# Performance work log

Measured on AMD Instinct MI355X. Metric: run time of the kernel, lower is better.

## Reference

```python
import jax, jax.numpy as jnp
import numpy as np

B, S, F, D, K = 4096, 64, 8, 64, 16  # batch_size, seq_len, input_size, d_model, knns


def setup_inputs() -> dict:
    key = jax.random.key(0)
    ks = jax.random.split(key, 3)
    return {
        "x": jax.random.normal(ks[0], (B, S, F), jnp.float32),
        "W_emb": jax.random.normal(ks[1], (F, D), jnp.float32) / np.sqrt(F),
        "b_emb": jnp.zeros((D,), jnp.float32),
        "W_proj": jax.random.normal(ks[2], (D, F), jnp.float32) / np.sqrt(D),
        "b_proj": jnp.zeros((F,), jnp.float32),
    }


def reference(x, W_emb, b_emb, W_proj, b_proj):
    # enc_embedding
    x_enc = x @ W_emb + b_emb                       # [B,S,D]
    x_re = x_enc.reshape(B, S * D)                  # flatten per sample
    # batch self-similarity
    attn = jnp.einsum('bl,cl->bc', x_re, x_re) / np.sqrt(D * S)
    diag = jnp.eye(B, dtype=bool)
    attn = jnp.where(diag, -jnp.inf, attn)
    scores = jax.nn.softmax(attn, axis=-1)          # [B,B]
    # einsum('bd,bc->bd', x_re, scores) == x_re * scores.sum(-1)
    x_rec = x_re * jnp.sum(scores, axis=-1, keepdims=True)
    x_rec = x_rec.reshape(B, S, D)
    x_rec_proj = x_rec @ W_proj + b_proj            # [B,S,F]
    # top-k neighbor gather
    _, top_idx = jax.lax.top_k(scores, K)           # [B,K] int32
    gathered = x_rec_proj[top_idx]                  # [B,K,S,F]
    diff_1 = jnp.mean(jnp.diff(gathered, axis=1) ** 2)
    diff_2 = jnp.mean(jnp.diff(gathered, axis=2) ** 2)
    loss = jnp.mean((x_rec_proj - x) ** 2) + diff_1 + diff_2  # var == 2
    return loss, x_rec_proj
```

## Files before the change

### kernel.cpp

```cpp
#include <hip/hip_runtime.h>
#include <math.h>

#define NB 4096
#define NS 64
#define NF 8
#define ND 64
#define KL 512
#define NK 16

typedef _Float16 half8 __attribute__((ext_vector_type(8)));
typedef float    f32x4 __attribute__((ext_vector_type(4)));

#define GLD16(src, dst) \
  __builtin_amdgcn_global_load_lds((const __attribute__((address_space(1))) void*)(src), \
                                   (__attribute__((address_space(3))) void*)(dst), 16, 0, 0)

#define WAITVM(N) asm volatile("s_waitcnt vmcnt(" #N ")" ::: "memory")

__device__ __forceinline__ unsigned short f2bf_rne(float f) {
    unsigned v = __float_as_uint(f);
    return (unsigned short)((v + 0x7FFFu + ((v >> 16) & 1u)) >> 16);
}
__device__ __forceinline__ unsigned bf16key(float v, int col) {
    const unsigned u = f2bf_rne(v);
    const unsigned s = (u & 0x8000u) ? (~u & 0xFFFFu) : (u | 0x8000u);
    return (s << 12) | (unsigned)(4095 - col);
}

#define UPD2(M1, M2, K) { const unsigned k_ = (K); \
    if (k_ > M1) { M2 = M1; M1 = k_; } else if (k_ > M2) M2 = k_; }

__device__ __forceinline__ float blk_reduce(float v, float* red) {
    #pragma unroll
    for (int o = 32; o > 0; o >>= 1) v += __shfl_down(v, o, 64);
    const int t = threadIdx.x;
    __syncthreads();
    if ((t & 63) == 0) red[t >> 6] = v;
    __syncthreads();
    float r = 0.f;
    if (t == 0) r = red[0] + red[1] + red[2] + red[3];
    return r;
}

__global__ __launch_bounds__(64) void consts_kernel(
    const float* __restrict__ Wemb, const float* __restrict__ bemb,
    const float* __restrict__ Wp, const float* __restrict__ bp,
    float* __restrict__ cst, double* __restrict__ acc)
{
    __shared__ float sWe[NF * ND];
    __shared__ float sWp[ND * NF];
    __shared__ float sbe[ND];
    __shared__ float sbp[NF];
    const int t = threadIdx.x;
    #pragma unroll
    for (int i = 0; i < 12; ++i) acc[t + i * 64] = 0.0;
    #pragma unroll
    for (int i = 0; i < 8; ++i) { sWe[t + i * 64] = Wemb[t + i * 64]; sWp[t + i * 64] = Wp[t + i * 64]; }
    sbe[t] = bemb[t];
    if (t < NF) sbp[t] = bp[t];
    __syncthreads();
    const int f = t >> 3, f2 = t & 7;
    float g = 0.f, m = 0.f;
    #pragma unroll
    for (int d = 0; d < ND; ++d) {
        g += sWe[f * ND + d] * sWe[f2 * ND + d];
        m += sWe[f * ND + d] * sWp[d * NF + f2];
    }
    cst[t] = g;
    cst[64 + t] = m;
    if (t < NF) {
        float uu = 0.f, cc = 0.f;
        #pragma unroll
        for (int d = 0; d < ND; ++d) {
            uu += sWe[t * ND + d] * sbe[d];
            cc += sbe[d] * sWp[d * NF + t];
        }
        cst[128 + t] = uu;
        cst[136 + t] = cc + sbp[t];
    }
}

__global__ __launch_bounds__(256) void prep_kernel(
    const float* __restrict__ x, const float* __restrict__ cst,
    _Float16* __restrict__ X16, _Float16* __restrict__ Y16,
    float* __restrict__ proj, float* __restrict__ r, double* __restrict__ acc)
{
    __shared__ float sG[64], sM[64], su[8], sc[8];
    __shared__ float red[4];
    const int t = threadIdx.x, lane = t & 63, w = t >> 6;
    if (t < 64) sG[t] = cst[t];
    else if (t < 128) sM[t - 64] = cst[t];
    else if (t < 136) su[t - 128] = cst[t];
    else if (t < 144) sc[t - 136] = cst[t];
    __syncthreads();
    const int b = blockIdx.x * 4 + w;
    const size_t base = (size_t)b * KL + lane * 8;
    const f32x4 x0 = *(const f32x4*)&x[base];
    const f32x4 x1 = *(const f32x4*)&x[base + 4];
    float xv[8] = {x0[0], x0[1], x0[2], x0[3], x1[0], x1[1], x1[2], x1[3]};
    float yv[8], pv[8];
    #pragma unroll
    for (int f2 = 0; f2 < 8; ++f2) { yv[f2] = 0.f; pv[f2] = sc[f2]; }
    #pragma unroll
    for (int f = 0; f < 8; ++f)
        #pragma unroll
        for (int f2 = 0; f2 < 8; ++f2) {
            yv[f2] += xv[f] * sG[f * 8 + f2];
            pv[f2] += xv[f] * sM[f * 8 + f2];
        }
    half8 hx, hy;
    #pragma unroll
    for (int j = 0; j < 8; ++j) { hx[j] = (_Float16)xv[j]; hy[j] = (_Float16)yv[j]; }
    *(half8*)&X16[base] = hx;
    *(half8*)&Y16[base] = hy;
    *(f32x4*)&proj[base] = (f32x4){pv[0], pv[1], pv[2], pv[3]};
    *(f32x4*)&proj[base + 4] = (f32x4){pv[4], pv[5], pv[6], pv[7]};
    float rv = 0.f;
    #pragma unroll
    for (int f = 0; f < 8; ++f) rv += xv[f] * su[f];
    #pragma unroll
    for (int o = 32; o > 0; o >>= 1) rv += __shfl_down(rv, o, 64);
    if (lane == 0) r[b] = rv;
    float s1 = 0.f;
    #pragma unroll
    for (int j = 0; j < 8; ++j) { const float d = pv[j] - xv[j]; s1 += d * d; }
    const float tot = blk_reduce(s1, red);
    if (t == 0) atomicAdd(&acc[(size_t)(blockIdx.x & 31) * 8], (double)tot);
}

__global__ __launch_bounds__(256) void attn_gemm_kernel(
    const _Float16* __restrict__ Xf, const _Float16* __restrict__ Yf,
    const float* __restrict__ rvec, unsigned* __restrict__ cand)
{
    __shared__ __align__(16) char smem_raw[49152];
    _Float16* smem = (_Float16*)smem_raw;

    const int t = threadIdx.x;
    const int lane = t & 63, wid = t >> 6;
    const int wr = wid >> 1, wc = wid & 1;

    const int bid0 = blockIdx.x;
    const int bid = (bid0 & 7) * 128 + (bid0 >> 3);
    const int it = bid >> 5, jt = bid & 31;
    const int i0 = it * 128, j0 = jt * 128;

    f32x4 acc[4][4];
    #pragma unroll
    for (int m = 0; m < 4; ++m)
        #pragma unroll
        for (int n = 0; n < 4; ++n) acc[m][n] = (f32x4){0.f, 0.f, 0.f, 0.f};

    const int lrow = lane & 15, g = lane >> 4;
    const int ksw = (g ^ ((lrow >> 1) & 3)) * 8;

    const int c0 = t, c1 = t + 256;
    const int r0 = c0 >> 2, r1 = c1 >> 2;
    const int cs0 = ((c0 & 3) ^ ((r0 >> 1) & 3)) * 8;
    const int cs1 = ((c1 & 3) ^ ((r1 >> 1) & 3)) * 8;
    const _Float16* pa0 = Xf + (size_t)(i0 + r0) * KL + cs0;
    const _Float16* pa1 = Xf + (size_t)(i0 + r1) * KL + cs1;
    const _Float16* pb0 = Yf + (size_t)(j0 + r0) * KL + cs0;
    const _Float16* pb1 = Yf + (size_t)(j0 + r1) * KL + cs1;
    _Float16* d0 = smem + c0 * 8;
    _Float16* d1 = smem + c1 * 8;

#define STG(BUF, KH) { \
    GLD16(pa0 + (KH), d0 + (BUF) * 8192); \
    GLD16(pa1 + (KH), d1 + (BUF) * 8192); \
    GLD16(pb0 + (KH), d0 + (BUF) * 8192 + 4096); \
    GLD16(pb1 + (KH), d1 + (BUF) * 8192 + 4096); }

    const int roA = wr * 2048 + lrow * 32 + ksw;
    const int roB = wc * 2048 + lrow * 32 + ksw;

#define COMPUTE(BUF) { \
    const _Float16* sA = smem + (BUF) * 8192; \
    const _Float16* sB = sA + 4096; \
    half8 fa[4], fb[4]; \
    _Pragma("unroll") \
    for (int m = 0; m < 4; ++m) { \
        fa[m] = *(const half8*)&sA[roA + m * 512]; \
        fb[m] = *(const half8*)&sB[roB + m * 512]; \
    } \
    __builtin_amdgcn_s_setprio(1); \
    _Pragma("unroll") \
    for (int m = 0; m < 4; ++m) \
        _Pragma("unroll") \
        for (int n = 0; n < 4; ++n) \
            acc[m][n] = __builtin_amdgcn_mfma_f32_16x16x32_f16(fa[m], fb[n], acc[m][n], 0, 0, 0); \
    __builtin_amdgcn_s_setprio(0); }

    STG(0, 0); STG(1, 32);
    pa0 += 64; pa1 += 64; pb0 += 64; pb1 += 64;
    #pragma unroll 1
    for (int io = 0; io < 4; ++io) {
        WAITVM(4); __builtin_amdgcn_s_barrier(); STG(2, 0);  COMPUTE(0);
        WAITVM(4); __builtin_amdgcn_s_barrier(); STG(0, 32); COMPUTE(1);
        WAITVM(4); __builtin_amdgcn_s_barrier(); STG(1, 64); COMPUTE(2);
        pa0 += 96; pa1 += 96; pb0 += 96; pb1 += 96;
    }
    WAITVM(4); __builtin_amdgcn_s_barrier(); STG(2, 0);  COMPUTE(0);
    WAITVM(4); __builtin_amdgcn_s_barrier(); STG(0, 32); COMPUTE(1);
    WAITVM(4); __builtin_amdgcn_s_barrier(); COMPUTE(2);
    WAITVM(0); __builtin_amdgcn_s_barrier(); COMPUTE(0);
#undef STG
#undef COMPUTE

    const int diag = (it == jt);

    float rj[4];
    #pragma unroll
    for (int n = 0; n < 4; ++n) rj[n] = rvec[j0 + wc * 64 + n * 16 + lrow];

    uint2* dp = (uint2*)smem_raw;

    __syncthreads();

    #pragma unroll
    for (int m = 0; m < 4; ++m)
        #pragma unroll
        for (int rr = 0; rr < 4; ++rr) {
            const int rl = wr * 64 + m * 16 + g * 4 + rr;
            const int i  = i0 + rl;
            unsigned m1 = 0u, m2 = 0u;
            #pragma unroll
            for (int n = 0; n < 4; ++n) {
                const int j = j0 + wc * 64 + n * 16 + lrow;
                unsigned key = bf16key(acc[m][n][rr] + rj[n], j);
                if (diag && i == j) key = 0u;
                UPD2(m1, m2, key)
            }
            uint2 pr; pr.x = m1; pr.y = m2;
            dp[(rl * 2 + wc) * 17 + lrow] = pr;
        }

    __syncthreads();

    {
        const int rl = t >> 1, p = t & 1;
        unsigned m1 = 0u, m2 = 0u;
        #pragma unroll
        for (int l = 0; l < 16; ++l) {
            const uint2 pr = dp[(rl * 2 + p) * 17 + l];
            UPD2(m1, m2, pr.x) UPD2(m1, m2, pr.y)
        }
        uint2 st; st.x = m1; st.y = m2;
        *(uint2*)(cand + (size_t)(i0 + rl) * 128 + (size_t)(jt * 2 + p) * 2) = st;
    }
}

__global__ __launch_bounds__(256) void topk_diffs_kernel(
    const unsigned* __restrict__ cand, const float* __restrict__ proj,
    double* __restrict__ acc)
{
    const int t = threadIdx.x, lane = t & 63, w = t >> 6;
    const int b = blockIdx.x * 4 + w;
    const uint2 kk = *(const uint2*)(cand + (size_t)b * 128 + lane * 2);
    unsigned k0 = kk.x, k1 = kk.y;

    float s1 = 0.f, s2 = 0.f;
    float prev[8];

    for (int k = 0; k < NK; ++k) {
        unsigned bv = k0 > k1 ? k0 : k1;
        #pragma unroll
        for (int o = 1; o <= 32; o <<= 1)
            bv = max(bv, (unsigned)__shfl_xor((int)bv, o, 64));
        const int idx = 4095 - (int)(bv & 0xFFFu);

        const float* pp = proj + (size_t)idx * 512 + lane * 8;
        const f32x4 a0 = *(const f32x4*)pp;
        const f32x4 a1 = *(const f32x4*)(pp + 4);
        float cur[8] = {a0[0], a0[1], a0[2], a0[3], a1[0], a1[1], a1[2], a1[3]};
        if (k) {
            #pragma unroll
            for (int j = 0; j < 8; ++j) { const float d = cur[j] - prev[j]; s1 += d * d; }
        }
        if (lane < 63) {
            const f32x4 n0 = *(const f32x4*)(pp + 8);
            const f32x4 n1 = *(const f32x4*)(pp + 12);
            const float nxt[8] = {n0[0], n0[1], n0[2], n0[3], n1[0], n1[1], n1[2], n1[3]};
            #pragma unroll
            for (int j = 0; j < 8; ++j) { const float d = nxt[j] - cur[j]; s2 += d * d; }
        }
        #pragma unroll
        for (int j = 0; j < 8; ++j) prev[j] = cur[j];

        if (k0 == bv) k0 = 0u;
        if (k1 == bv) k1 = 0u;
    }

    #pragma unroll
    for (int o = 32; o > 0; o >>= 1) { s1 += __shfl_down(s1, o, 64); s2 += __shfl_down(s2, o, 64); }
    if (lane == 0) {
        const size_t slot = (size_t)(blockIdx.x & 31) * 8;
        atomicAdd(&acc[(size_t)32 * 8 + slot], (double)s1);
        atomicAdd(&acc[(size_t)64 * 8 + slot], (double)s2);
    }
}

__global__ void finalize_kernel(const double* __restrict__ acc, float* __restrict__ out) {
    if (threadIdx.x == 0) {
        double s0 = 0.0, s1 = 0.0, s2 = 0.0;
        #pragma unroll
        for (int i = 0; i < 32; ++i) {
            s0 += acc[(size_t)i * 8];
            s1 += acc[(size_t)(32 + i) * 8];
            s2 += acc[(size_t)(64 + i) * 8];
        }
        out[0] = (float)(s0 / 2097152.0 + s1 / 31457280.0 + s2 / 33030144.0);
    }
}

extern "C" void kernel_launch(void* const* d_in, const int* in_sizes, int n_in,
                              void* d_out, int out_size, void* d_ws, size_t ws_size,
                              hipStream_t stream) {
    const float* x    = (const float*)d_in[0];
    const float* Wemb = (const float*)d_in[1];
    const float* bemb = (const float*)d_in[2];
    const float* Wp   = (const float*)d_in[3];
    const float* bp   = (const float*)d_in[4];
    float* out  = (float*)d_out;
    float* proj = out + 1;

    char* ws = (char*)d_ws;
    _Float16* X16 = (_Float16*)ws;
    _Float16* Y16 = (_Float16*)(ws + ((size_t)4 << 20));
    unsigned* cand = (unsigned*)(ws + ((size_t)8 << 20));
    float*  cst   = (float*)(ws + ((size_t)10 << 20));
    float*  rvec  = (float*)(ws + ((size_t)10 << 20) + 4096);
    double* acc   = (double*)(ws + ((size_t)10 << 20) + 65536);

    consts_kernel<<<1, 64, 0, stream>>>(Wemb, bemb, Wp, bp, cst, acc);
    prep_kernel<<<NB / 4, 256, 0, stream>>>(x, cst, X16, Y16, proj, rvec, acc);
    attn_gemm_kernel<<<1024, 256, 0, stream>>>(X16, Y16, rvec, cand);
    topk_diffs_kernel<<<NB / 4, 256, 0, stream>>>(cand, proj, acc);
    finalize_kernel<<<1, 64, 0, stream>>>(acc, out);
}
```

Before: 69.59 us.

## Fuse constants into prep, shrink GEMM tiles, replace atomics with per-block partials

Folds the one-block constants kernel into every prep block, which recomputes the small Gram and projection matrices redundantly but removes a launch. The attention GEMM moves from 128x128 to 128x64 tiles, with 2048 blocks, less LDS and three loads per stage, and drops the setprio hints. Top-2 keys now come from fp32 bits truncated to 20 bits instead of bf16 rounding. Global double atomics are replaced by per-block partial sums that a parallel finalize kernel reduces, trading atomic contention for an extra read of 3072 doubles.

```diff
diff --git a/kernel.cpp b/kernel.cpp
--- a/kernel.cpp
+++ b/kernel.cpp
@@ -17,14 +17,10 @@
 
 #define WAITVM(N) asm volatile("s_waitcnt vmcnt(" #N ")" ::: "memory")
 
-__device__ __forceinline__ unsigned short f2bf_rne(float f) {
-    unsigned v = __float_as_uint(f);
-    return (unsigned short)((v + 0x7FFFu + ((v >> 16) & 1u)) >> 16);
-}
-__device__ __forceinline__ unsigned bf16key(float v, int col) {
-    const unsigned u = f2bf_rne(v);
-    const unsigned s = (u & 0x8000u) ? (~u & 0xFFFFu) : (u | 0x8000u);
-    return (s << 12) | (unsigned)(4095 - col);
+__device__ __forceinline__ unsigned f32key(float v, int col) {
+    const unsigned u = __float_as_uint(v);
+    const unsigned s = ((int)u < 0) ? ~u : (u | 0x80000000u);
+    return (s & 0xFFFFF000u) | (unsigned)(4095 - col);
 }
 
 #define UPD2(M1, M2, K) { const unsigned k_ = (K); \
@@ -42,57 +38,43 @@
     return r;
 }
 
-__global__ __launch_bounds__(64) void consts_kernel(
-    const float* __restrict__ Wemb, const float* __restrict__ bemb,
-    const float* __restrict__ Wp, const float* __restrict__ bp,
-    float* __restrict__ cst, double* __restrict__ acc)
+__global__ __launch_bounds__(256) void prep_kernel(
+    const float* __restrict__ x, const float* __restrict__ Wemb,
+    const float* __restrict__ bemb, const float* __restrict__ Wp,
+    const float* __restrict__ bp,
+    _Float16* __restrict__ X16, _Float16* __restrict__ Y16,
+    float* __restrict__ proj, float* __restrict__ r, double* __restrict__ p1)
 {
-    __shared__ float sWe[NF * ND];
-    __shared__ float sWp[ND * NF];
-    __shared__ float sbe[ND];
-    __shared__ float sbp[NF];
-    const int t = threadIdx.x;
-    #pragma unroll
-    for (int i = 0; i < 12; ++i) acc[t + i * 64] = 0.0;
-    #pragma unroll
-    for (int i = 0; i < 8; ++i) { sWe[t + i * 64] = Wemb[t + i * 64]; sWp[t + i * 64] = Wp[t + i * 64]; }
-    sbe[t] = bemb[t];
-    if (t < NF) sbp[t] = bp[t];
-    __syncthreads();
-    const int f = t >> 3, f2 = t & 7;
-    float g = 0.f, m = 0.f;
-    #pragma unroll
-    for (int d = 0; d < ND; ++d) {
-        g += sWe[f * ND + d] * sWe[f2 * ND + d];
-        m += sWe[f * ND + d] * sWp[d * NF + f2];
-    }
-    cst[t] = g;
-    cst[64 + t] = m;
-    if (t < NF) {
+    __shared__ float sWe[512], sWp[512], sbe[64], sbp[8];
+    __shared__ float sG[64], sM[64], su[8], sc[8];
+    __shared__ float red[4];
+    const int t = threadIdx.x, lane = t & 63, w = t >> 6;
+    sWe[t] = Wemb[t]; sWe[t + 256] = Wemb[t + 256];
+    sWp[t] = Wp[t];   sWp[t + 256] = Wp[t + 256];
+    if (t < 64) sbe[t] = bemb[t];
+    if (t < 8)  sbp[t] = bp[t];
+    __syncthreads();
+    if (t < 64) {
+        const int f = t >> 3, f2 = t & 7;
+        float g = 0.f, m = 0.f;
+        #pragma unroll
+        for (int d = 0; d < ND; ++d) {
+            g += sWe[f * ND + d] * sWe[f2 * ND + d];
+            m += sWe[f * ND + d] * sWp[d * NF + f2];
+        }
+        sG[t] = g; sM[t] = m;
+    }
+    if (t < 8) {
         float uu = 0.f, cc = 0.f;
         #pragma unroll
         for (int d = 0; d < ND; ++d) {
             uu += sWe[t * ND + d] * sbe[d];
             cc += sbe[d] * sWp[d * NF + t];
         }
-        cst[128 + t] = uu;
-        cst[136 + t] = cc + sbp[t];
-    }
-}
-
-__global__ __launch_bounds__(256) void prep_kernel(
-    const float* __restrict__ x, const float* __restrict__ cst,
-    _Float16* __restrict__ X16, _Float16* __restrict__ Y16,
-    float* __restrict__ proj, float* __restrict__ r, double* __restrict__ acc)
-{
-    __shared__ float sG[64], sM[64], su[8], sc[8];
-    __shared__ float red[4];
-    const int t = threadIdx.x, lane = t & 63, w = t >> 6;
-    if (t < 64) sG[t] = cst[t];
-    else if (t < 128) sM[t - 64] = cst[t];
-    else if (t < 136) su[t - 128] = cst[t];
-    else if (t < 144) sc[t - 136] = cst[t];
-    __syncthreads();
+        su[t] = uu; sc[t] = cc + sbp[t];
+    }
+    __syncthreads();
+
     const int b = blockIdx.x * 4 + w;
     const size_t base = (size_t)b * KL + lane * 8;
     const f32x4 x0 = *(const f32x4*)&x[base];
@@ -125,134 +107,127 @@
     #pragma unroll
     for (int j = 0; j < 8; ++j) { const float d = pv[j] - xv[j]; s1 += d * d; }
     const float tot = blk_reduce(s1, red);
-    if (t == 0) atomicAdd(&acc[(size_t)(blockIdx.x & 31) * 8], (double)tot);
+    if (t == 0) p1[blockIdx.x] = (double)tot;
 }
 
 __global__ __launch_bounds__(256) void attn_gemm_kernel(
     const _Float16* __restrict__ Xf, const _Float16* __restrict__ Yf,
     const float* __restrict__ rvec, unsigned* __restrict__ cand)
 {
-    __shared__ __align__(16) char smem_raw[49152];
+    __shared__ __align__(16) char smem_raw[36864];
     _Float16* smem = (_Float16*)smem_raw;
 
     const int t = threadIdx.x;
     const int lane = t & 63, wid = t >> 6;
-    const int wr = wid >> 1, wc = wid & 1;
 
     const int bid0 = blockIdx.x;
-    const int bid = (bid0 & 7) * 128 + (bid0 >> 3);
-    const int it = bid >> 5, jt = bid & 31;
-    const int i0 = it * 128, j0 = jt * 128;
-
-    f32x4 acc[4][4];
-    #pragma unroll
-    for (int m = 0; m < 4; ++m)
+    const int bid = (bid0 & 7) * 256 + (bid0 >> 3);
+    const int it = bid >> 6, jt = bid & 63;
+    const int i0 = it * 128, j0 = jt * 64;
+
+    f32x4 acc[2][4];
+    #pragma unroll
+    for (int m = 0; m < 2; ++m)
         #pragma unroll
         for (int n = 0; n < 4; ++n) acc[m][n] = (f32x4){0.f, 0.f, 0.f, 0.f};
 
     const int lrow = lane & 15, g = lane >> 4;
     const int ksw = (g ^ ((lrow >> 1) & 3)) * 8;
 
-    const int c0 = t, c1 = t + 256;
-    const int r0 = c0 >> 2, r1 = c1 >> 2;
-    const int cs0 = ((c0 & 3) ^ ((r0 >> 1) & 3)) * 8;
-    const int cs1 = ((c1 & 3) ^ ((r1 >> 1) & 3)) * 8;
-    const _Float16* pa0 = Xf + (size_t)(i0 + r0) * KL + cs0;
-    const _Float16* pa1 = Xf + (size_t)(i0 + r1) * KL + cs1;
-    const _Float16* pb0 = Yf + (size_t)(j0 + r0) * KL + cs0;
-    const _Float16* pb1 = Yf + (size_t)(j0 + r1) * KL + cs1;
-    _Float16* d0 = smem + c0 * 8;
-    _Float16* d1 = smem + c1 * 8;
+    const int rA0 = t >> 2,         cA0 = t & 3;
+    const int rA1 = (t + 256) >> 2, cA1 = t & 3;
+    const int csA0 = (cA0 ^ ((rA0 >> 1) & 3)) * 8;
+    const int csA1 = (cA1 ^ ((rA1 >> 1) & 3)) * 8;
+    const int csB  = csA0;
+    const _Float16* pA0 = Xf + (size_t)(i0 + rA0) * KL + csA0;
+    const _Float16* pA1 = Xf + (size_t)(i0 + rA1) * KL + csA1;
+    const _Float16* pB  = Yf + (size_t)(j0 + rA0) * KL + csB;
+    _Float16* dA0 = smem + t * 8;
+    _Float16* dA1 = smem + (t + 256) * 8;
+    _Float16* dB  = smem + 4096 + t * 8;
 
 #define STG(BUF, KH) { \
-    GLD16(pa0 + (KH), d0 + (BUF) * 8192); \
-    GLD16(pa1 + (KH), d1 + (BUF) * 8192); \
-    GLD16(pb0 + (KH), d0 + (BUF) * 8192 + 4096); \
-    GLD16(pb1 + (KH), d1 + (BUF) * 8192 + 4096); }
-
-    const int roA = wr * 2048 + lrow * 32 + ksw;
-    const int roB = wc * 2048 + lrow * 32 + ksw;
+    GLD16(pA0 + (KH), dA0 + (BUF) * 6144); \
+    GLD16(pA1 + (KH), dA1 + (BUF) * 6144); \
+    GLD16(pB  + (KH), dB  + (BUF) * 6144); }
+
+    const int roA = wid * 1024 + lrow * 32 + ksw;
+    const int roB = lrow * 32 + ksw;
 
 #define COMPUTE(BUF) { \
-    const _Float16* sA = smem + (BUF) * 8192; \
-    const _Float16* sB = sA + 4096; \
-    half8 fa[4], fb[4]; \
+    const _Float16* sA = smem + (BUF) * 6144 + roA; \
+    const _Float16* sB = smem + (BUF) * 6144 + 4096 + roB; \
+    half8 fa[2], fb[4]; \
     _Pragma("unroll") \
-    for (int m = 0; m < 4; ++m) { \
-        fa[m] = *(const half8*)&sA[roA + m * 512]; \
-        fb[m] = *(const half8*)&sB[roB + m * 512]; \
-    } \
-    __builtin_amdgcn_s_setprio(1); \
+    for (int m = 0; m < 2; ++m) fa[m] = *(const half8*)&sA[m * 512]; \
     _Pragma("unroll") \
-    for (int m = 0; m < 4; ++m) \
+    for (int n = 0; n < 4; ++n) fb[n] = *(const half8*)&sB[n * 512]; \
+    _Pragma("unroll") \
+    for (int m = 0; m < 2; ++m) \
         _Pragma("unroll") \
         for (int n = 0; n < 4; ++n) \
-            acc[m][n] = __builtin_amdgcn_mfma_f32_16x16x32_f16(fa[m], fb[n], acc[m][n], 0, 0, 0); \
-    __builtin_amdgcn_s_setprio(0); }
+            acc[m][n] = __builtin_amdgcn_mfma_f32_16x16x32_f16(fa[m], fb[n], acc[m][n], 0, 0, 0); }
 
     STG(0, 0); STG(1, 32);
-    pa0 += 64; pa1 += 64; pb0 += 64; pb1 += 64;
+    pA0 += 64; pA1 += 64; pB += 64;
     #pragma unroll 1
     for (int io = 0; io < 4; ++io) {
-        WAITVM(4); __builtin_amdgcn_s_barrier(); STG(2, 0);  COMPUTE(0);
-        WAITVM(4); __builtin_amdgcn_s_barrier(); STG(0, 32); COMPUTE(1);
-        WAITVM(4); __builtin_amdgcn_s_barrier(); STG(1, 64); COMPUTE(2);
-        pa0 += 96; pa1 += 96; pb0 += 96; pb1 += 96;
-    }
-    WAITVM(4); __builtin_amdgcn_s_barrier(); STG(2, 0);  COMPUTE(0);
-    WAITVM(4); __builtin_amdgcn_s_barrier(); STG(0, 32); COMPUTE(1);
-    WAITVM(4); __builtin_amdgcn_s_barrier(); COMPUTE(2);
+        WAITVM(3); __builtin_amdgcn_s_barrier(); STG(2, 0);  COMPUTE(0);
+        WAITVM(3); __builtin_amdgcn_s_barrier(); STG(0, 32); COMPUTE(1);
+        WAITVM(3); __builtin_amdgcn_s_barrier(); STG(1, 64); COMPUTE(2);
+        pA0 += 96; pA1 += 96; pB += 96;
+    }
+    WAITVM(3); __builtin_amdgcn_s_barrier(); STG(2, 0);  COMPUTE(0);
+    WAITVM(3); __builtin_amdgcn_s_barrier(); STG(0, 32); COMPUTE(1);
+    WAITVM(3); __builtin_amdgcn_s_barrier(); COMPUTE(2);
     WAITVM(0); __builtin_amdgcn_s_barrier(); COMPUTE(0);
 #undef STG
 #undef COMPUTE
 
-    const int diag = (it == jt);
-
     float rj[4];
     #pragma unroll
-    for (int n = 0; n < 4; ++n) rj[n] = rvec[j0 + wc * 64 + n * 16 + lrow];
+    for (int n = 0; n < 4; ++n) rj[n] = rvec[j0 + n * 16 + lrow];
 
     uint2* dp = (uint2*)smem_raw;
-
-    __syncthreads();
-
-    #pragma unroll
-    for (int m = 0; m < 4; ++m)
+    __syncthreads();
+
+    #pragma unroll
+    for (int m = 0; m < 2; ++m)
         #pragma unroll
         for (int rr = 0; rr < 4; ++rr) {
-            const int rl = wr * 64 + m * 16 + g * 4 + rr;
+            const int rl = wid * 32 + m * 16 + g * 4 + rr;
             const int i  = i0 + rl;
             unsigned m1 = 0u, m2 = 0u;
             #pragma unroll
             for (int n = 0; n < 4; ++n) {
-                const int j = j0 + wc * 64 + n * 16 + lrow;
-                unsigned key = bf16key(acc[m][n][rr] + rj[n], j);
-                if (diag && i == j) key = 0u;
+                const int j = j0 + n * 16 + lrow;
+                unsigned key = f32key(acc[m][n][rr] + rj[n], j);
+                if (i == j) key = 0u;
                 UPD2(m1, m2, key)
             }
             uint2 pr; pr.x = m1; pr.y = m2;
-            dp[(rl * 2 + wc) * 17 + lrow] = pr;
-        }
-
-    __syncthreads();
-
-    {
-        const int rl = t >> 1, p = t & 1;
+            dp[rl * 17 + lrow] = pr;
+        }
+
+    __syncthreads();
+
+    if (t < 128) {
         unsigned m1 = 0u, m2 = 0u;
         #pragma unroll
         for (int l = 0; l < 16; ++l) {
-            const uint2 pr = dp[(rl * 2 + p) * 17 + l];
+            const uint2 pr = dp[t * 17 + l];
             UPD2(m1, m2, pr.x) UPD2(m1, m2, pr.y)
         }
         uint2 st; st.x = m1; st.y = m2;
-        *(uint2*)(cand + (size_t)(i0 + rl) * 128 + (size_t)(jt * 2 + p) * 2) = st;
+        *(uint2*)(cand + (size_t)(i0 + t) * 128 + (size_t)jt * 2) = st;
     }
 }
 
 __global__ __launch_bounds__(256) void topk_diffs_kernel(
     const unsigned* __restrict__ cand, const float* __restrict__ proj,
-    double* __restrict__ acc)
+    double* __restrict__ p2, double* __restrict__ p3)
 {
+    __shared__ double bs1[4], bs2[4];
     const int t = threadIdx.x, lane = t & 63, w = t >> 6;
     const int b = blockIdx.x * 4 + w;
     const uint2 kk = *(const uint2*)(cand + (size_t)b * 128 + lane * 2);
@@ -292,24 +267,30 @@
 
     #pragma unroll
     for (int o = 32; o > 0; o >>= 1) { s1 += __shfl_down(s1, o, 64); s2 += __shfl_down(s2, o, 64); }
-    if (lane == 0) {
-        const size_t slot = (size_t)(blockIdx.x & 31) * 8;
-        atomicAdd(&acc[(size_t)32 * 8 + slot], (double)s1);
-        atomicAdd(&acc[(size_t)64 * 8 + slot], (double)s2);
-    }
-}
-
-__global__ void finalize_kernel(const double* __restrict__ acc, float* __restrict__ out) {
-    if (threadIdx.x == 0) {
-        double s0 = 0.0, s1 = 0.0, s2 = 0.0;
-        #pragma unroll
-        for (int i = 0; i < 32; ++i) {
-            s0 += acc[(size_t)i * 8];
-            s1 += acc[(size_t)(32 + i) * 8];
-            s2 += acc[(size_t)(64 + i) * 8];
-        }
-        out[0] = (float)(s0 / 2097152.0 + s1 / 31457280.0 + s2 / 33030144.0);
-    }
+    if (lane == 0) { bs1[w] = (double)s1; bs2[w] = (double)s2; }
+    __syncthreads();
+    if (t == 0) {
+        p2[blockIdx.x] = bs1[0] + bs1[1] + bs1[2] + bs1[3];
+        p3[blockIdx.x] = bs2[0] + bs2[1] + bs2[2] + bs2[3];
+    }
+}
+
+__global__ __launch_bounds__(256) void finalize_kernel(
+    const double* __restrict__ p1, const double* __restrict__ p2,
+    const double* __restrict__ p3, float* __restrict__ out)
+{
+    __shared__ double dred[4];
+    const int t = threadIdx.x, lane = t & 63, w = t >> 6;
+    double v = 0.0;
+    for (int i = t; i < 1024; i += 256)
+        v += p1[i] * (1.0 / 2097152.0)
+           + p2[i] * (1.0 / 31457280.0)
+           + p3[i] * (1.0 / 33030144.0);
+    #pragma unroll
+    for (int o = 32; o > 0; o >>= 1) v += __shfl_down(v, o, 64);
+    if (lane == 0) dred[w] = v;
+    __syncthreads();
+    if (t == 0) out[0] = (float)(dred[0] + dred[1] + dred[2] + dred[3]);
 }
 
 extern "C" void kernel_launch(void* const* d_in, const int* in_sizes, int n_in,
@@ -327,13 +308,13 @@
     _Float16* X16 = (_Float16*)ws;
     _Float16* Y16 = (_Float16*)(ws + ((size_t)4 << 20));
     unsigned* cand = (unsigned*)(ws + ((size_t)8 << 20));
-    float*  cst   = (float*)(ws + ((size_t)10 << 20));
-    float*  rvec  = (float*)(ws + ((size_t)10 << 20) + 4096);
-    double* acc   = (double*)(ws + ((size_t)10 << 20) + 65536);
-
-    consts_kernel<<<1, 64, 0, stream>>>(Wemb, bemb, Wp, bp, cst, acc);
-    prep_kernel<<<NB / 4, 256, 0, stream>>>(x, cst, X16, Y16, proj, rvec, acc);
-    attn_gemm_kernel<<<1024, 256, 0, stream>>>(X16, Y16, rvec, cand);
-    topk_diffs_kernel<<<NB / 4, 256, 0, stream>>>(cand, proj, acc);
-    finalize_kernel<<<1, 64, 0, stream>>>(acc, out);
-}
+    float*  rvec  = (float*)(ws + ((size_t)10 << 20));
+    double* p1    = (double*)(ws + ((size_t)10 << 20) + 65536);
+    double* p2    = p1 + 1024;
+    double* p3    = p2 + 1024;
+
+    prep_kernel<<<NB / 4, 256, 0, stream>>>(x, Wemb, bemb, Wp, bp, X16, Y16, proj, rvec, p1);
+    attn_gemm_kernel<<<2048, 256, 0, stream>>>(X16, Y16, rvec, cand);
+    topk_diffs_kernel<<<NB / 4, 256, 0, stream>>>(cand, proj, p2, p3);
+    finalize_kernel<<<1, 256, 0, stream>>>(p1, p2, p3, out);
+}
```

Result: faster. 66.92 us (-3.8%).
